# Optimization experiments

Hardware: AMD Instinct MI355X
Metric: run time of the kernel (lower is better)

The kernel has to match this reference:

```python
import jax, jax.numpy as jnp
import numpy as np


def setup_inputs() -> dict:
    key = jax.random.key(0)
    k1, _ = jax.random.split(key)
    x = jax.random.normal(k1, (2, 16, 16, 16, 64), dtype=jnp.float32)
    gamma = jnp.ones((1,), dtype=jnp.float32)  # learned scalar (zeros at init; ones to make output nontrivial)
    return {"x": x, "gamma": gamma}


def reference(x, gamma):
    # x: (B, D, H, W, C); faithful to the Keras layer: flatten spatial dims,
    # energy = Q @ Q^T over the N=D*H*W axis, softmax(axis=-1), attn @ Q,
    # then gamma-scaled residual add.
    B, D, H, W, C = x.shape
    N = D * H * W
    q = x.reshape(B, N, C)                            # proj_query (B, N, C)
    energy = jnp.einsum('bnc,bmc->bnm', q, q)          # (B, N, N)
    attn = jax.nn.softmax(energy, axis=-1)
    out = jnp.einsum('bnm,bmc->bnc', attn, q)          # (B, N, C)
    out = out.reshape(B, D, H, W, C)
    return gamma * out + x
```

## Files before the change

kernel.cpp:

```cpp
#include <hip/hip_runtime.h>
#include <hip/hip_bf16.h>
#include <math.h>


#define NN 4096
#define CC 64
#define LOG2E 1.4426950408889634f

typedef __attribute__((ext_vector_type(4))) float f32x4;
typedef __attribute__((ext_vector_type(8))) short bf16x8;
typedef __attribute__((ext_vector_type(4))) short bf16x4;
typedef unsigned short u16;
typedef __attribute__((ext_vector_type(4))) u16 u16x4;
typedef __attribute__((ext_vector_type(2))) unsigned u32x2;

__device__ inline u16 f2bf(float f) {
  union { float f; unsigned u; } v; v.f = f;
  unsigned r = (v.u + 0x7fffu + ((v.u >> 16) & 1u)) >> 16;
  return (u16)r;
}
__device__ inline float bf2f(short h) {
  union { unsigned u; float f; } v;
  v.u = ((unsigned)(unsigned short)h) << 16;
  return v.f;
}
__device__ inline unsigned fbits(float f) {
  union { float f; unsigned u; } v; v.f = f;
  return v.u;
}
__device__ inline bf16x8 cvt8(f32x4 a, f32x4 b) {
  bf16x8 r;
  r[0] = (short)f2bf(a[0]); r[1] = (short)f2bf(a[1]);
  r[2] = (short)f2bf(a[2]); r[3] = (short)f2bf(a[3]);
  r[4] = (short)f2bf(b[0]); r[5] = (short)f2bf(b[1]);
  r[6] = (short)f2bf(b[2]); r[7] = (short)f2bf(b[3]);
  return r;
}

__global__ __launch_bounds__(256) void prep_kernel(const float* __restrict__ x,
                                                   u16* __restrict__ Qb,
                                                   u16* __restrict__ Vt) {
  __shared__ u16 t[64][20];
  int b = blockIdx.x >> 8;
  int n0 = (blockIdx.x & 255) << 4;
  const f32x4* x4 = (const f32x4*)(x + ((size_t)b * NN + n0) * CC);
  u16* qb = Qb + ((size_t)b * NN + n0) * CC;
  {
    int idx4 = threadIdx.x;
    int i = idx4 >> 4, cg = idx4 & 15;
    f32x4 v = x4[idx4];
    u16x4 h;
    h[0] = f2bf(v[0]); h[1] = f2bf(v[1]); h[2] = f2bf(v[2]); h[3] = f2bf(v[3]);
    *(u16x4*)(qb + (size_t)i * CC + cg * 4) = h;
    t[cg * 4 + 0][i] = h[0]; t[cg * 4 + 1][i] = h[1];
    t[cg * 4 + 2][i] = h[2]; t[cg * 4 + 3][i] = h[3];
  }
  __syncthreads();
  int kb = n0 >> 6, kw0 = n0 & 63;
  {
    int idx4 = threadIdx.x;
    int c = idx4 >> 2, i4 = (idx4 & 3) * 4;
    u16x4 h = *(const u16x4*)(&t[c][i4]);
    *(u16x4*)(Vt + (((size_t)b * (NN / 64) + kb) * 64 + c) * 64 + kw0 + i4) = h;
  }
}

template <int S>
__global__ __launch_bounds__(256, 8) void attn_split(
    const u16* __restrict__ Qb, const u16* __restrict__ Vt,
    u16* __restrict__ Opart, float* __restrict__ lpart) {
  constexpr int KPS = NN / S;
  constexpr int ITERS = KPS / 32;
  const int w = threadIdx.x >> 6;
  const int lane = threadIdx.x & 63;
  const int quad = lane >> 4, col = lane & 15;
  const int blk = blockIdx.x;
  const int b = blk / (64 * S);
  const int rg = (blk / S) & 63;
  const int s = blk % S;

  __shared__ u16 KL[2][32 * 32];
  __shared__ u16 KH[2][32 * 32];
  __shared__ u16 VT[2][64 * 32];
  __shared__ u16 PB[4][16 * 32];

  const u16* Qbase = Qb + (size_t)b * NN * CC;
  const u16* Vbase = Vt + (size_t)b * NN * CC;
  const int row0 = rg * 64 + w * 16;

  bf16x8 qs0, qs1;
  float m_sc;
  {
    const u16* qp = Qbase + (size_t)(row0 + col) * CC + quad * 8;
    bf16x8 r0 = *(const bf16x8*)qp;
    bf16x8 r1 = *(const bf16x8*)(qp + 32);
    float msum = 0.f;
#pragma unroll
    for (int j = 0; j < 8; ++j) {
      float a0 = bf2f(r0[j]), a1 = bf2f(r1[j]);
      u16 h0 = f2bf(a0 * LOG2E), h1 = f2bf(a1 * LOG2E);
      qs0[j] = (short)h0; qs1[j] = (short)h1;
      msum += bf2f((short)h0) * a0 + bf2f((short)h1) * a1;
    }
    msum += __shfl_xor(msum, 16);
    msum += __shfl_xor(msum, 32);
    m_sc = msum;
  }

  f32x4 zero = {0.f, 0.f, 0.f, 0.f};
  f32x4 acc[4] = {zero, zero, zero, zero};
  f32x4 accl = zero;
  f32x4 cinit = {-m_sc, -m_sc, -m_sc, -m_sc};
  bf16x8 onesb;
#pragma unroll
  for (int j = 0; j < 8; ++j) onesb[j] = (short)0x3F80;

  const int swz = (lane & 3) ^ ((lane >> 3) & 3);
  const int krow = (w & 1) * 16 + (lane >> 2);
  const int kch = (w >> 1) * 32;
  const int vrow = w * 16 + (lane >> 2);
  const u16* ksrc0 = Qbase + (size_t)(s * KPS + krow) * CC + kch + swz * 8;
  const u16* vsrc0 = Vbase + (size_t)(s * (KPS >> 6)) * 4096 + (size_t)vrow * 64 + swz * 8;
  u16* kdst = ((w >> 1) ? &KH[0][0] : &KL[0][0]) + (w & 1) * (16 * 32);
  u16* vdst = &VT[0][0] + w * (16 * 32);

#define STAGE(p, it)                                                          \
  {                                                                           \
    __builtin_amdgcn_global_load_lds(                                         \
        (const __attribute__((address_space(1))) unsigned*)(ksrc0 + (size_t)(it) * (32 * CC)), \
        (__attribute__((address_space(3))) unsigned*)(kdst + (p) * (32 * 32)),\
        16, 0, 0);                                                            \
    __builtin_amdgcn_global_load_lds(                                         \
        (const __attribute__((address_space(1))) unsigned*)(vsrc0 + ((it) >> 1) * 4096 + ((it) & 1) * 32), \
        (__attribute__((address_space(3))) unsigned*)(vdst + (p) * (64 * 32)),\
        16, 0, 0);                                                            \
  }

  STAGE(0, 0)
  STAGE(1, 1)
  const int cp = (col >> 1) & 3;
  u16* PBw = &PB[w][0];

#pragma unroll
  for (int i = 0; i < ITERS; ++i) {
    if (i + 1 < ITERS)
      asm volatile("s_waitcnt vmcnt(2)" ::: "memory");
    else
      asm volatile("s_waitcnt vmcnt(0)" ::: "memory");
    __builtin_amdgcn_sched_barrier(0);
    __builtin_amdgcn_s_barrier();
    __builtin_amdgcn_sched_barrier(0);
    const int p = i & 1;

    f32x4 sx[2];
    __builtin_amdgcn_s_setprio(1);
#pragma unroll
    for (int t = 0; t < 2; ++t) {
      bf16x8 ka = *(const bf16x8*)&KL[p][(t * 16 + col) * 32 + (quad ^ cp) * 8];
      bf16x8 kb = *(const bf16x8*)&KH[p][(t * 16 + col) * 32 + (quad ^ cp) * 8];
      sx[t] = __builtin_amdgcn_mfma_f32_16x16x32_bf16(ka, qs0, cinit, 0, 0, 0);
      sx[t] = __builtin_amdgcn_mfma_f32_16x16x32_bf16(kb, qs1, sx[t], 0, 0, 0);
    }
    __builtin_amdgcn_s_setprio(0);
#pragma unroll
    for (int t = 0; t < 2; ++t) {
      f32x4 pv;
#pragma unroll
      for (int r = 0; r < 4; ++r) pv[r] = exp2f(sx[t][r]);
      u32x2 d;
      d[0] = __builtin_amdgcn_perm(fbits(pv[1]), fbits(pv[0]), 0x07060302u);
      d[1] = __builtin_amdgcn_perm(fbits(pv[3]), fbits(pv[2]), 0x07060302u);
      *(u32x2*)&PBw[col * 32 + ((t * 2 + (quad >> 1)) ^ cp) * 8 + (quad & 1) * 4] = d;
    }
    bf16x8 pf0 = *(const bf16x8*)&PBw[col * 32 + (quad ^ cp) * 8];
    __builtin_amdgcn_s_setprio(1);
    accl = __builtin_amdgcn_mfma_f32_16x16x32_bf16(pf0, onesb, accl, 0, 0, 0);
#pragma unroll
    for (int cg = 0; cg < 4; ++cg) {
      bf16x8 va = *(const bf16x8*)&VT[p][(cg * 16 + col) * 32 + (quad ^ cp) * 8];
      acc[cg] = __builtin_amdgcn_mfma_f32_16x16x32_bf16(pf0, va, acc[cg], 0, 0, 0);
    }
    __builtin_amdgcn_s_setprio(0);
    __builtin_amdgcn_sched_barrier(0);
    __builtin_amdgcn_s_barrier();
    __builtin_amdgcn_sched_barrier(0);
    if (i + 2 < ITERS) STAGE(p, i + 2)
  }
#undef STAGE

  size_t pbase = (((size_t)(b * 64 + rg)) * S + s) * (64 * 64);
  size_t lbase = (((size_t)(b * 64 + rg)) * S + s) * 64;
  if (col == 0) {
#pragma unroll
    for (int r = 0; r < 4; ++r) lpart[lbase + w * 16 + quad * 4 + r] = accl[r];
  }
#pragma unroll
  for (int r = 0; r < 4; ++r) {
    int lr = w * 16 + quad * 4 + r;
    size_t o = pbase + (size_t)lr * 64;
    Opart[o + col]      = f2bf(acc[0][r]);
    Opart[o + col + 16] = f2bf(acc[1][r]);
    Opart[o + col + 32] = f2bf(acc[2][r]);
    Opart[o + col + 48] = f2bf(acc[3][r]);
  }
}

template <int S>
__global__ __launch_bounds__(256) void epi_kernel(
    const float* __restrict__ x, const float* __restrict__ gamma,
    const u16* __restrict__ Opart, const float* __restrict__ lpart,
    float* __restrict__ out) {
  int t = blockIdx.x * 256 + threadIdx.x;
  int cg = t & 15;
  int n = (t >> 4) & (NN - 1);
  int b = t >> 16;
  int rb = n >> 6, lr = n & 63;
  size_t obase = ((size_t)(b * 64 + rb) * S) * 4096 + (size_t)lr * 64 + cg * 4;
  size_t lbase = ((size_t)(b * 64 + rb) * S) * 64 + lr;
  f32x4 sO = {0.f, 0.f, 0.f, 0.f};
  float sL = 0.f;
#pragma unroll
  for (int s = 0; s < S; ++s) {
    u16x4 o4 = *(const u16x4*)(Opart + obase + (size_t)s * 4096);
    sL += lpart[lbase + s * 64];
    sO[0] += bf2f((short)o4[0]); sO[1] += bf2f((short)o4[1]);
    sO[2] += bf2f((short)o4[2]); sO[3] += bf2f((short)o4[3]);
  }
  size_t xi = (((size_t)b * NN + n) * CC + cg * 4);
  f32x4 xv = *(const f32x4*)(x + xi);
  float g = gamma[0], inv = 1.f / sL;
  f32x4 ov;
#pragma unroll
  for (int j = 0; j < 4; ++j) ov[j] = g * (sO[j] * inv) + xv[j];
  *(f32x4*)(((float*)out) + xi) = ov;
}

template <int WPB>
__global__ __launch_bounds__(WPB * 64, 4) void attn_fast(
    const float* __restrict__ x, const float* __restrict__ gamma,
    const u16* __restrict__ Qb, const u16* __restrict__ Vt,
    float* __restrict__ out) {
  const int w = threadIdx.x >> 6;
  const int lane = threadIdx.x & 63;
  const int quad = lane >> 4, col = lane & 15;
  const int b = blockIdx.x >> 8;
  const int tile = (blockIdx.x & 255) << 4;

  extern __shared__ char smem[];
  float* Osh = (float*)smem;
  float* lsh = Osh + WPB * 1024;
  u16* pl = (u16*)(lsh + WPB * 16) + w * 2176;

  const size_t xoff = (size_t)b * NN * CC;
  const u16* Qbase = Qb + xoff;
  const u16* Vbase = Vt + xoff;

  bf16x8 qf0 = *(const bf16x8*)(Qbase + (size_t)(tile + col) * CC + quad * 8);
  bf16x8 qf1 = *(const bf16x8*)(Qbase + (size_t)(tile + col) * CC + 32 + quad * 8);

  float msum = 0.f;
#pragma unroll
  for (int j = 0; j < 8; ++j) {
    float a = bf2f(qf0[j]), c = bf2f(qf1[j]);
    msum += a * a + c * c;
  }
  msum += __shfl_xor(msum, 16);
  msum += __shfl_xor(msum, 32);
  float m_i[4];
#pragma unroll
  for (int r = 0; r < 4; ++r) m_i[r] = __shfl(msum, quad * 4 + r);

  f32x4 zero = {0.f, 0.f, 0.f, 0.f};
  f32x4 acc[4] = {zero, zero, zero, zero};
  float l_i[4] = {0.f, 0.f, 0.f, 0.f};

  const int k0 = w * (NN / WPB);
#pragma unroll 2
  for (int kt = k0; kt < k0 + NN / WPB; kt += 64) {
    u16* plc = pl + ((kt >> 6) & 1) * 1088;
    f32x4 sx[4];
#pragma unroll
    for (int t = 0; t < 4; ++t) {
      const u16* kp = Qbase + (size_t)(kt + t * 16 + col) * CC + quad * 8;
      bf16x8 ka = *(const bf16x8*)kp;
      bf16x8 kb = *(const bf16x8*)(kp + 32);
      sx[t] = __builtin_amdgcn_mfma_f32_16x16x32_bf16(qf0, ka, zero, 0, 0, 0);
      sx[t] = __builtin_amdgcn_mfma_f32_16x16x32_bf16(qf1, kb, sx[t], 0, 0, 0);
    }
#pragma unroll
    for (int t = 0; t < 4; ++t) {
#pragma unroll
      for (int r = 0; r < 4; ++r) {
        float p = __expf(sx[t][r] - m_i[r]);
        l_i[r] += p;
        plc[(quad * 4 + r) * 68 + t * 16 + col] = f2bf(p);
      }
    }
    bf16x8 pf0 = *(const bf16x8*)(plc + col * 68 + quad * 8);
    bf16x8 pf1 = *(const bf16x8*)(plc + col * 68 + 32 + quad * 8);
#pragma unroll
    for (int cg = 0; cg < 4; ++cg) {
      const u16* vp = Vbase + (((size_t)(kt >> 6)) * 64 + cg * 16 + col) * 64 + quad * 8;
      bf16x8 v0 = *(const bf16x8*)vp;
      bf16x8 v1 = *(const bf16x8*)(vp + 32);
      acc[cg] = __builtin_amdgcn_mfma_f32_16x16x32_bf16(pf0, v0, acc[cg], 0, 0, 0);
      acc[cg] = __builtin_amdgcn_mfma_f32_16x16x32_bf16(pf1, v1, acc[cg], 0, 0, 0);
    }
  }

#pragma unroll
  for (int r = 0; r < 4; ++r)
#pragma unroll
    for (int off = 1; off < 16; off <<= 1) l_i[r] += __shfl_xor(l_i[r], off, 16);
#pragma unroll
  for (int r = 0; r < 4; ++r) {
    int row = quad * 4 + r;
    Osh[(w * 16 + row) * 64 + col]      = acc[0][r];
    Osh[(w * 16 + row) * 64 + col + 16] = acc[1][r];
    Osh[(w * 16 + row) * 64 + col + 32] = acc[2][r];
    Osh[(w * 16 + row) * 64 + col + 48] = acc[3][r];
    if (col == 0) lsh[w * 16 + row] = l_i[r];
  }
  __syncthreads();

  float g = gamma[0];
  for (int row = w; row < 16; row += WPB) {
    float L = 0.f, val = 0.f;
#pragma unroll
    for (int w2 = 0; w2 < WPB; ++w2) {
      L += lsh[w2 * 16 + row];
      val += Osh[(w2 * 16 + row) * 64 + lane];
    }
    size_t o = xoff + (size_t)(tile + row) * CC + lane;
    out[o] = g * (val / L) + x[o];
  }
}

template <int WPB>
__global__ __launch_bounds__(512) void attn_fb(const float* __restrict__ x,
                                               const float* __restrict__ gamma,
                                               float* __restrict__ out) {
  const int w = threadIdx.x >> 6;
  const int lane = threadIdx.x & 63;
  const int quad = lane >> 4, col = lane & 15;
  const int b = blockIdx.x >> 8;
  const int tile = (blockIdx.x & 255) << 4;

  extern __shared__ char smem[];
  float* Osh = (float*)smem;
  float* msh = Osh + WPB * 1024;
  float* lsh = msh + WPB * 16;
  u16* pl = (u16*)(lsh + WPB * 16) + w * 768;
  u16* vt = (u16*)(lsh + WPB * 16) + WPB * 768 + w * 2176;

  const size_t xoff = (size_t)b * NN * CC;
  const f32x4* x4 = (const f32x4*)(x + xoff);

  bf16x8 qf0, qf1;
  {
    int ri = (tile + col) * 16 + quad * 2;
    qf0 = cvt8(x4[ri], x4[ri + 1]);
    qf1 = cvt8(x4[ri + 8], x4[ri + 9]);
  }
  f32x4 zero = {0.f, 0.f, 0.f, 0.f};
  f32x4 acc0 = zero, acc1 = zero, acc2 = zero, acc3 = zero;
  float m_i[4], l_i[4];
#pragma unroll
  for (int r = 0; r < 4; ++r) { m_i[r] = -1e30f; l_i[r] = 0.f; }

  const int k0 = w * (NN / WPB);
  for (int kt = k0; kt < k0 + NN / WPB; kt += 32) {
    bf16x8 k00, k01, k10, k11;
    {
      int kb = (kt + col) * 16 + quad * 2;
      k00 = cvt8(x4[kb], x4[kb + 1]);
      k01 = cvt8(x4[kb + 8], x4[kb + 9]);
      k10 = cvt8(x4[kb + 256], x4[kb + 257]);
      k11 = cvt8(x4[kb + 264], x4[kb + 265]);
#pragma unroll
      for (int h = 0; h < 2; ++h) {
        bf16x8 va = h ? k10 : k00, vb = h ? k11 : k01;
        int base = (h * 16 + col) * 68 + quad * 8;
        *(bf16x4*)(vt + base) = __builtin_shufflevector(va, va, 0, 1, 2, 3);
        *(bf16x4*)(vt + base + 4) = __builtin_shufflevector(va, va, 4, 5, 6, 7);
        *(bf16x4*)(vt + base + 32) = __builtin_shufflevector(vb, vb, 0, 1, 2, 3);
        *(bf16x4*)(vt + base + 36) = __builtin_shufflevector(vb, vb, 4, 5, 6, 7);
      }
    }
    f32x4 s0 = zero, s1 = zero;
    s0 = __builtin_amdgcn_mfma_f32_16x16x32_bf16(qf0, k00, s0, 0, 0, 0);
    s0 = __builtin_amdgcn_mfma_f32_16x16x32_bf16(qf1, k01, s0, 0, 0, 0);
    s1 = __builtin_amdgcn_mfma_f32_16x16x32_bf16(qf0, k10, s1, 0, 0, 0);
    s1 = __builtin_amdgcn_mfma_f32_16x16x32_bf16(qf1, k11, s1, 0, 0, 0);

    float p0[4], p1[4], alpha[4];
#pragma unroll
    for (int r = 0; r < 4; ++r) {
      float mx = fmaxf(s0[r], s1[r]);
#pragma unroll
      for (int off = 1; off < 16; off <<= 1) mx = fmaxf(mx, __shfl_xor(mx, off, 16));
      float mn = fmaxf(m_i[r], mx);
      alpha[r] = __expf(m_i[r] - mn);
      p0[r] = __expf(s0[r] - mn);
      p1[r] = __expf(s1[r] - mn);
      float rs = p0[r] + p1[r];
#pragma unroll
      for (int off = 1; off < 16; off <<= 1) rs += __shfl_xor(rs, off, 16);
      l_i[r] = l_i[r] * alpha[r] + rs;
      m_i[r] = mn;
    }
#pragma unroll
    for (int r = 0; r < 4; ++r) {
      acc0[r] *= alpha[r]; acc1[r] *= alpha[r];
      acc2[r] *= alpha[r]; acc3[r] *= alpha[r];
    }
#pragma unroll
    for (int r = 0; r < 4; ++r) {
      pl[(quad * 4 + r) * 24 + col] = f2bf(p0[r]);
      pl[384 + (quad * 4 + r) * 24 + col] = f2bf(p1[r]);
    }
    bf16x8 pf = *(const bf16x8*)(pl + (quad >> 1) * 384 + col * 24 + (quad & 1) * 8);

    bf16x8 v0, v1, v2, v3;
#pragma unroll
    for (int j = 0; j < 8; ++j) {
      int rb = (quad * 8 + j) * 68 + col;
      v0[j] = (short)vt[rb];
      v1[j] = (short)vt[rb + 16];
      v2[j] = (short)vt[rb + 32];
      v3[j] = (short)vt[rb + 48];
    }
    acc0 = __builtin_amdgcn_mfma_f32_16x16x32_bf16(pf, v0, acc0, 0, 0, 0);
    acc1 = __builtin_amdgcn_mfma_f32_16x16x32_bf16(pf, v1, acc1, 0, 0, 0);
    acc2 = __builtin_amdgcn_mfma_f32_16x16x32_bf16(pf, v2, acc2, 0, 0, 0);
    acc3 = __builtin_amdgcn_mfma_f32_16x16x32_bf16(pf, v3, acc3, 0, 0, 0);
  }

#pragma unroll
  for (int r = 0; r < 4; ++r) {
    int row = quad * 4 + r;
    Osh[(w * 16 + row) * 64 + col] = acc0[r];
    Osh[(w * 16 + row) * 64 + col + 16] = acc1[r];
    Osh[(w * 16 + row) * 64 + col + 32] = acc2[r];
    Osh[(w * 16 + row) * 64 + col + 48] = acc3[r];
    if (col == 0) { msh[w * 16 + row] = m_i[r]; lsh[w * 16 + row] = l_i[r]; }
  }
  __syncthreads();

  float g = gamma[0];
  for (int row = w; row < 16; row += WPB) {
    float M = -1e30f;
#pragma unroll
    for (int w2 = 0; w2 < WPB; ++w2) M = fmaxf(M, msh[w2 * 16 + row]);
    float L = 0.f, val = 0.f;
#pragma unroll
    for (int w2 = 0; w2 < WPB; ++w2) {
      float e = __expf(msh[w2 * 16 + row] - M);
      L += lsh[w2 * 16 + row] * e;
      val += Osh[(w2 * 16 + row) * 64 + lane] * e;
    }
    size_t o = xoff + (size_t)(tile + row) * CC + lane;
    out[o] = g * (val / L) + x[o];
  }
}

extern "C" void kernel_launch(void* const* d_in, const int* in_sizes, int n_in,
                              void* d_out, int out_size, void* d_ws, size_t ws_size,
                              hipStream_t stream) {
  const float* x = (const float*)d_in[0];
  const float* gamma = (const float*)d_in[1];
  float* out = (float*)d_out;

  constexpr int S = 16;
  constexpr size_t kQV = (size_t)2 * 2 * NN * CC * sizeof(u16);
  constexpr size_t kOp = (size_t)2 * 64 * S * 64 * 64 * sizeof(u16);
  constexpr size_t kLp = (size_t)2 * 64 * S * 64 * sizeof(float);
  if (ws_size >= kQV + kOp + kLp) {
    u16* Qb = (u16*)d_ws;
    u16* Vt = Qb + (size_t)2 * NN * CC;
    u16* Opart = (u16*)((char*)d_ws + kQV);
    float* lpart = (float*)((char*)d_ws + kQV + kOp);
    prep_kernel<<<512, 256, 0, stream>>>(x, Qb, Vt);
    attn_split<S><<<2 * 64 * S, 256, 0, stream>>>(Qb, Vt, Opart, lpart);
    epi_kernel<S><<<(2 * NN * 16) / 256, 256, 0, stream>>>(x, gamma, Opart, lpart, out);
  } else if (ws_size >= kQV) {
    u16* Qb = (u16*)d_ws;
    u16* Vt = Qb + (size_t)2 * NN * CC;
    prep_kernel<<<512, 256, 0, stream>>>(x, Qb, Vt);
    constexpr int SM = 8 * 1024 * 4 + 8 * 16 * 4 + 8 * 2176 * 2;
    attn_fast<8><<<512, 512, SM, stream>>>(x, gamma, Qb, Vt, out);
  } else {
    constexpr int SM4 = 4 * (1024 + 32) * 4 + 4 * 768 * 2 + 4 * 2176 * 2;
    attn_fb<4><<<512, 256, SM4, stream>>>(x, gamma, out);
  }
}
```

Before: 83.83 us.

## Switch split attention to 32x32x16 MFMA with register-shuffled P and intra-block K-split

Rewrites the split-KV attention kernel to use 32x32x16 bf16 MFMAs over 64-key tiles. Each pair of waves splits the keys of a 32-row query tile, and the partial outputs are reduced through LDS before vectorized stores. The P matrix is converted with v_cvt_pk_bf16 and rearranged through cross-lane shuffles instead of an LDS round trip, and row sums are accumulated in registers instead of by a ones-MFMA. The split count drops from 16 to 8 and the occupancy hint from 8 to 4, which halves the partial buffers and epilogue reduction work but gives fewer blocks and a longer serial loop per block.

```diff
diff --git a/kernel.cpp b/kernel.cpp
--- a/kernel.cpp
+++ b/kernel.cpp
@@ -8,10 +8,12 @@
 #define LOG2E 1.4426950408889634f
 
 typedef __attribute__((ext_vector_type(4))) float f32x4;
+typedef __attribute__((ext_vector_type(16))) float f32x16;
 typedef __attribute__((ext_vector_type(8))) short bf16x8;
 typedef __attribute__((ext_vector_type(4))) short bf16x4;
 typedef unsigned short u16;
 typedef __attribute__((ext_vector_type(4))) u16 u16x4;
+typedef __attribute__((ext_vector_type(8))) u16 u16x8;
 typedef __attribute__((ext_vector_type(2))) unsigned u32x2;
 
 __device__ inline u16 f2bf(float f) {
@@ -27,6 +29,11 @@
 __device__ inline unsigned fbits(float f) {
   union { float f; unsigned u; } v; v.f = f;
   return v.u;
+}
+__device__ inline unsigned cvtpk(float lo, float hi) {
+  unsigned d;
+  asm("v_cvt_pk_bf16_f32 %0, %1, %2" : "=v"(d) : "v"(lo), "v"(hi));
+  return d;
 }
 __device__ inline bf16x8 cvt8(f32x4 a, f32x4 b) {
   bf16x8 r;
@@ -66,119 +73,142 @@
 }
 
 template <int S>
-__global__ __launch_bounds__(256, 8) void attn_split(
+__global__ __launch_bounds__(256, 4) void attn_split(
     const u16* __restrict__ Qb, const u16* __restrict__ Vt,
     u16* __restrict__ Opart, float* __restrict__ lpart) {
   constexpr int KPS = NN / S;
-  constexpr int ITERS = KPS / 32;
+  constexpr int ITERS = KPS / 64;
+  const int lane = threadIdx.x & 63;
   const int w = threadIdx.x >> 6;
-  const int lane = threadIdx.x & 63;
-  const int quad = lane >> 4, col = lane & 15;
+  const int wk = w & 1, wr2 = w >> 1;
+  const int hf = lane >> 5, l31 = lane & 31, c8 = lane & 7;
   const int blk = blockIdx.x;
   const int b = blk / (64 * S);
   const int rg = (blk / S) & 63;
   const int s = blk % S;
 
-  __shared__ u16 KL[2][32 * 32];
-  __shared__ u16 KH[2][32 * 32];
-  __shared__ u16 VT[2][64 * 32];
-  __shared__ u16 PB[4][16 * 32];
+  __shared__ __align__(16) char smem[32768];
+  u16* KT = (u16*)smem;
+  u16* VT = (u16*)(smem + 16384);
 
   const u16* Qbase = Qb + (size_t)b * NN * CC;
   const u16* Vbase = Vt + (size_t)b * NN * CC;
-  const int row0 = rg * 64 + w * 16;
-
-  bf16x8 qs0, qs1;
+  const int row0 = rg * 64 + wr2 * 32;
+
+  bf16x8 qs[4];
   float m_sc;
   {
-    const u16* qp = Qbase + (size_t)(row0 + col) * CC + quad * 8;
-    bf16x8 r0 = *(const bf16x8*)qp;
-    bf16x8 r1 = *(const bf16x8*)(qp + 32);
+    const u16* qp = Qbase + (size_t)(row0 + l31) * CC + hf * 8;
     float msum = 0.f;
 #pragma unroll
-    for (int j = 0; j < 8; ++j) {
-      float a0 = bf2f(r0[j]), a1 = bf2f(r1[j]);
-      u16 h0 = f2bf(a0 * LOG2E), h1 = f2bf(a1 * LOG2E);
-      qs0[j] = (short)h0; qs1[j] = (short)h1;
-      msum += bf2f((short)h0) * a0 + bf2f((short)h1) * a1;
-    }
-    msum += __shfl_xor(msum, 16);
+    for (int sl = 0; sl < 4; ++sl) {
+      bf16x8 r0 = *(const bf16x8*)(qp + sl * 16);
+      bf16x8 t;
+#pragma unroll
+      for (int j = 0; j < 8; ++j) {
+        float a = bf2f(r0[j]);
+        u16 hs = f2bf(a * LOG2E);
+        t[j] = (short)hs;
+        msum += bf2f((short)hs) * a;
+      }
+      qs[sl] = t;
+    }
     msum += __shfl_xor(msum, 32);
     m_sc = msum;
   }
 
-  f32x4 zero = {0.f, 0.f, 0.f, 0.f};
-  f32x4 acc[4] = {zero, zero, zero, zero};
-  f32x4 accl = zero;
-  f32x4 cinit = {-m_sc, -m_sc, -m_sc, -m_sc};
-  bf16x8 onesb;
-#pragma unroll
-  for (int j = 0; j < 8; ++j) onesb[j] = (short)0x3F80;
-
-  const int swz = (lane & 3) ^ ((lane >> 3) & 3);
-  const int krow = (w & 1) * 16 + (lane >> 2);
-  const int kch = (w >> 1) * 32;
-  const int vrow = w * 16 + (lane >> 2);
-  const u16* ksrc0 = Qbase + (size_t)(s * KPS + krow) * CC + kch + swz * 8;
-  const u16* vsrc0 = Vbase + (size_t)(s * (KPS >> 6)) * 4096 + (size_t)vrow * 64 + swz * 8;
-  u16* kdst = ((w >> 1) ? &KH[0][0] : &KL[0][0]) + (w & 1) * (16 * 32);
-  u16* vdst = &VT[0][0] + w * (16 * 32);
+  f32x16 cinit;
+#pragma unroll
+  for (int r = 0; r < 16; ++r) cinit[r] = -m_sc;
+  f32x16 zero16;
+#pragma unroll
+  for (int r = 0; r < 16; ++r) zero16[r] = 0.f;
+  f32x16 acc[2] = {zero16, zero16};
+  float l_loc = 0.f;
+
+  const int g8 = lane >> 3;
+  const int swz = c8 ^ g8;
+  const u16* kptr = Qbase + (size_t)(s * KPS + w * 16 + g8) * CC + swz * 8;
+  const u16* vptr = Vbase + (size_t)(s * (KPS >> 6)) * 4096 + (size_t)(w * 16 + g8) * 64 + swz * 8;
 
 #define STAGE(p, it)                                                          \
   {                                                                           \
     __builtin_amdgcn_global_load_lds(                                         \
-        (const __attribute__((address_space(1))) unsigned*)(ksrc0 + (size_t)(it) * (32 * CC)), \
-        (__attribute__((address_space(3))) unsigned*)(kdst + (p) * (32 * 32)),\
-        16, 0, 0);                                                            \
+        (const __attribute__((address_space(1))) unsigned*)(kptr + (size_t)(it) * 4096),       \
+        (__attribute__((address_space(3))) unsigned*)&KT[(p) * 4096 + (w * 16) * 64], 16, 0, 0); \
     __builtin_amdgcn_global_load_lds(                                         \
-        (const __attribute__((address_space(1))) unsigned*)(vsrc0 + ((it) >> 1) * 4096 + ((it) & 1) * 32), \
-        (__attribute__((address_space(3))) unsigned*)(vdst + (p) * (64 * 32)),\
-        16, 0, 0);                                                            \
+        (const __attribute__((address_space(1))) unsigned*)(kptr + (size_t)(it) * 4096 + 512), \
+        (__attribute__((address_space(3))) unsigned*)&KT[(p) * 4096 + (w * 16 + 8) * 64], 16, 0, 0); \
+    __builtin_amdgcn_global_load_lds(                                         \
+        (const __attribute__((address_space(1))) unsigned*)(vptr + (size_t)(it) * 4096),       \
+        (__attribute__((address_space(3))) unsigned*)&VT[(p) * 4096 + (w * 16) * 64], 16, 0, 0); \
+    __builtin_amdgcn_global_load_lds(                                         \
+        (const __attribute__((address_space(1))) unsigned*)(vptr + (size_t)(it) * 4096 + 512), \
+        (__attribute__((address_space(3))) unsigned*)&VT[(p) * 4096 + (w * 16 + 8) * 64], 16, 0, 0); \
   }
 
   STAGE(0, 0)
   STAGE(1, 1)
-  const int cp = (col >> 1) & 3;
-  u16* PBw = &PB[w][0];
 
 #pragma unroll
   for (int i = 0; i < ITERS; ++i) {
     if (i + 1 < ITERS)
-      asm volatile("s_waitcnt vmcnt(2)" ::: "memory");
+      asm volatile("s_waitcnt vmcnt(4)" ::: "memory");
     else
       asm volatile("s_waitcnt vmcnt(0)" ::: "memory");
     __builtin_amdgcn_sched_barrier(0);
     __builtin_amdgcn_s_barrier();
     __builtin_amdgcn_sched_barrier(0);
     const int p = i & 1;
-
-    f32x4 sx[2];
+    const u16* KTp = KT + p * 4096;
+    const u16* VTp = VT + p * 4096;
+
+    f32x16 sx = cinit;
     __builtin_amdgcn_s_setprio(1);
 #pragma unroll
-    for (int t = 0; t < 2; ++t) {
-      bf16x8 ka = *(const bf16x8*)&KL[p][(t * 16 + col) * 32 + (quad ^ cp) * 8];
-      bf16x8 kb = *(const bf16x8*)&KH[p][(t * 16 + col) * 32 + (quad ^ cp) * 8];
-      sx[t] = __builtin_amdgcn_mfma_f32_16x16x32_bf16(ka, qs0, cinit, 0, 0, 0);
-      sx[t] = __builtin_amdgcn_mfma_f32_16x16x32_bf16(kb, qs1, sx[t], 0, 0, 0);
+    for (int sl = 0; sl < 4; ++sl) {
+      bf16x8 kf = *(const bf16x8*)&KTp[(wk * 32 + l31) * 64 + ((sl * 2 + hf) ^ c8) * 8];
+      sx = __builtin_amdgcn_mfma_f32_32x32x16_bf16(kf, qs[sl], sx, 0, 0, 0);
     }
     __builtin_amdgcn_s_setprio(0);
-#pragma unroll
-    for (int t = 0; t < 2; ++t) {
-      f32x4 pv;
-#pragma unroll
-      for (int r = 0; r < 4; ++r) pv[r] = exp2f(sx[t][r]);
-      u32x2 d;
-      d[0] = __builtin_amdgcn_perm(fbits(pv[1]), fbits(pv[0]), 0x07060302u);
-      d[1] = __builtin_amdgcn_perm(fbits(pv[3]), fbits(pv[2]), 0x07060302u);
-      *(u32x2*)&PBw[col * 32 + ((t * 2 + (quad >> 1)) ^ cp) * 8 + (quad & 1) * 4] = d;
-    }
-    bf16x8 pf0 = *(const bf16x8*)&PBw[col * 32 + (quad ^ cp) * 8];
+
+    float p16[16];
+#pragma unroll
+    for (int r = 0; r < 16; ++r) p16[r] = exp2f(sx[r]);
+#pragma unroll
+    for (int r = 0; r < 16; ++r) l_loc += p16[r];
+    unsigned own[4][2], sh[4][2];
+#pragma unroll
+    for (int q = 0; q < 4; ++q) {
+      own[q][0] = cvtpk(p16[4 * q + 0], p16[4 * q + 1]);
+      own[q][1] = cvtpk(p16[4 * q + 2], p16[4 * q + 3]);
+    }
+#pragma unroll
+    for (int q = 0; q < 4; ++q) {
+      sh[q][0] = (unsigned)__shfl_xor((int)own[q][0], 32);
+      sh[q][1] = (unsigned)__shfl_xor((int)own[q][1], 32);
+    }
+    bf16x8 pf[2];
+#pragma unroll
+    for (int ks = 0; ks < 2; ++ks) {
+      unsigned d0 = hf ? sh[2 * ks + 1][0] : own[2 * ks][0];
+      unsigned d1 = hf ? sh[2 * ks + 1][1] : own[2 * ks][1];
+      unsigned d2 = hf ? own[2 * ks + 1][0] : sh[2 * ks][0];
+      unsigned d3 = hf ? own[2 * ks + 1][1] : sh[2 * ks][1];
+      bf16x8 f;
+      ((unsigned*)&f)[0] = d0; ((unsigned*)&f)[1] = d1;
+      ((unsigned*)&f)[2] = d2; ((unsigned*)&f)[3] = d3;
+      pf[ks] = f;
+    }
+
     __builtin_amdgcn_s_setprio(1);
-    accl = __builtin_amdgcn_mfma_f32_16x16x32_bf16(pf0, onesb, accl, 0, 0, 0);
-#pragma unroll
-    for (int cg = 0; cg < 4; ++cg) {
-      bf16x8 va = *(const bf16x8*)&VT[p][(cg * 16 + col) * 32 + (quad ^ cp) * 8];
-      acc[cg] = __builtin_amdgcn_mfma_f32_16x16x32_bf16(pf0, va, acc[cg], 0, 0, 0);
+#pragma unroll
+    for (int cg = 0; cg < 2; ++cg) {
+#pragma unroll
+      for (int ks = 0; ks < 2; ++ks) {
+        bf16x8 vf = *(const bf16x8*)&VTp[(cg * 32 + l31) * 64 + ((4 * wk + 2 * ks + hf) ^ c8) * 8];
+        acc[cg] = __builtin_amdgcn_mfma_f32_32x32x16_bf16(vf, pf[ks], acc[cg], 0, 0, 0);
+      }
     }
     __builtin_amdgcn_s_setprio(0);
     __builtin_amdgcn_sched_barrier(0);
@@ -188,21 +218,48 @@
   }
 #undef STAGE
 
-  size_t pbase = (((size_t)(b * 64 + rg)) * S + s) * (64 * 64);
+  l_loc += __shfl_xor(l_loc, 32);
+  float* LDSO = (float*)smem;
+  float* LDSL = (float*)(smem + 64 * 65 * 4);
+  const int qcol = wr2 * 32 + l31;
+  if (wk == 1) {
+#pragma unroll
+    for (int cg = 0; cg < 2; ++cg)
+#pragma unroll
+      for (int r = 0; r < 16; ++r) {
+        int ch = cg * 32 + (r & 3) + 8 * (r >> 2) + 4 * hf;
+        LDSO[ch * 65 + qcol] = acc[cg][r];
+      }
+  }
+  if (lane < 32) LDSL[wk * 64 + qcol] = l_loc;
+  __syncthreads();
+  if (wk == 0) {
+#pragma unroll
+    for (int cg = 0; cg < 2; ++cg)
+#pragma unroll
+      for (int r = 0; r < 16; ++r) {
+        int ch = cg * 32 + (r & 3) + 8 * (r >> 2) + 4 * hf;
+        LDSO[ch * 65 + qcol] += acc[cg][r];
+      }
+  }
+  __syncthreads();
+
+  size_t pbase = (((size_t)(b * 64 + rg)) * S + s) * 4096;
   size_t lbase = (((size_t)(b * 64 + rg)) * S + s) * 64;
-  if (col == 0) {
-#pragma unroll
-    for (int r = 0; r < 4; ++r) lpart[lbase + w * 16 + quad * 4 + r] = accl[r];
-  }
-#pragma unroll
-  for (int r = 0; r < 4; ++r) {
-    int lr = w * 16 + quad * 4 + r;
-    size_t o = pbase + (size_t)lr * 64;
-    Opart[o + col]      = f2bf(acc[0][r]);
-    Opart[o + col + 16] = f2bf(acc[1][r]);
-    Opart[o + col + 32] = f2bf(acc[2][r]);
-    Opart[o + col + 48] = f2bf(acc[3][r]);
-  }
+  {
+    int row = threadIdx.x >> 2;
+    int cq = threadIdx.x & 3;
+    u16x8 o0, o1;
+#pragma unroll
+    for (int j = 0; j < 8; ++j) {
+      o0[j] = f2bf(LDSO[(cq * 16 + j) * 65 + row]);
+      o1[j] = f2bf(LDSO[(cq * 16 + 8 + j) * 65 + row]);
+    }
+    *(u16x8*)(Opart + pbase + (size_t)row * 64 + cq * 16) = o0;
+    *(u16x8*)(Opart + pbase + (size_t)row * 64 + cq * 16 + 8) = o1;
+  }
+  if (threadIdx.x < 64)
+    lpart[lbase + threadIdx.x] = LDSL[threadIdx.x] + LDSL[64 + threadIdx.x];
 }
 
 template <int S>
@@ -471,7 +528,7 @@
   const float* gamma = (const float*)d_in[1];
   float* out = (float*)d_out;
 
-  constexpr int S = 16;
+  constexpr int S = 8;
   constexpr size_t kQV = (size_t)2 * 2 * NN * CC * sizeof(u16);
   constexpr size_t kOp = (size_t)2 * 64 * S * 64 * 64 * sizeof(u16);
   constexpr size_t kLp = (size_t)2 * 64 * S * 64 * sizeof(float);
```

New measurement: 82.29 us. Within noise of the previous version (-1.8%).
